# Optimization experiments

Measured on AMD Instinct MI355X. Metric: run time of the kernel, lower is better.

Reference implementation:

```python
import jax, jax.numpy as jnp
import numpy as np

# dims / constants (from init_kwargs and ParamsHP defaults)
N, C, TRS, SPT, BUF = 800, 64, 40, 10, 120
DT = 1e-4                      # step_size
A, OMEGA, G = -0.5, 10.0, 500.0
STD_IN, CY0, Y0_OFF, KG, KI = 100.0, 5.0, 2.0, 5.0, 1.0
T = TRS * SPT                  # total integration steps


def setup_inputs() -> dict:
    key = jax.random.key(0)
    k = jax.random.split(key, 7)
    external = jax.random.normal(k[0], (N, SPT, TRS), dtype=jnp.float32)
    hx = jax.random.uniform(k[1], (N, 2), dtype=jnp.float32)
    hE = jax.random.uniform(k[2], (N, BUF), dtype=jnp.float32)
    sc = jax.random.uniform(k[3], (N, N), dtype=jnp.float32)
    lm = jax.random.normal(k[4], (C, N), dtype=jnp.float32)
    noise_in = jax.random.normal(k[5], (T, N, 2), dtype=jnp.float32)
    # delays[i,j] = int(dist[i,j] / mu), bounded by buffer length
    delays = jax.random.randint(k[6], (N, N), 0, BUF, dtype=jnp.int64)
    return {"external": external, "hx": hx, "hE": hE, "sc": sc,
            "lm": lm, "noise_in": noise_in, "delays": delays}


def reference(external, hx, hE, sc, lm, noise_in, delays):
    # normalized structural connectivity and Laplacian diagonal term
    w = jnp.abs(sc)
    w_n = w / jnp.linalg.norm(w)          # (N,N)
    rowsum = jnp.sum(w_n, axis=1)         # (N,) -> dg = -diag(rowsum)
    jcol = jnp.broadcast_to(jnp.arange(N)[None, :], (N, N))
    # stimulus as (T, N): external is (N, steps_per_TR, TRs_per_window)
    ext = jnp.transpose(external, (2, 1, 0)).reshape(T, N)
    sqdt = jnp.sqrt(DT)

    def step(carry, inp):
        x, y, hEb = carry                 # x,y: (N,), hEb: (N,BUF)
        u, ns = inp                       # u: (N,), ns: (N,2)
        # delayed activity: Ed[i,j] = x_j(t - delays[i,j])
        Ed = hEb[jcol, delays]            # (N,N) irregular gather
        LEd = jnp.sum(w_n * Ed, axis=1)   # connectivity-weighted coupling
        r2 = x * x + y * y
        dx = (A - r2) * x - OMEGA * y + G * (LEd - rowsum * x) + KG * KI * u
        dy = (A - r2) * y + OMEGA * x
        x_new = x + DT * dx + sqdt * STD_IN * ns[:, 0]
        y_new = y + DT * dy + sqdt * STD_IN * ns[:, 1]
        hEb = jnp.concatenate([x_new[:, None], hEb[:, :-1]], axis=1)
        return (x_new, y_new, hEb), x_new

    (xf, yf, hEf), xs = jax.lax.scan(step, (hx[:, 0], hx[:, 1], hE), (ext, noise_in))
    # one EEG sample per TR (state at the last step of each TR)
    x_tr = xs.reshape(TRS, SPT, N)[:, -1, :]   # (TRS, N)
    eeg = CY0 * (x_tr @ lm.T) - Y0_OFF          # leadfield projection (TRS, C)
    return eeg.T                                # (C, TRS)
```

## Files before the change

### kernel.cpp

```cpp
#include <hip/hip_runtime.h>
#include <hip/hip_cooperative_groups.h>

namespace cg = cooperative_groups;

#define N_      800
#define C_      64
#define TRS_    40
#define SPT_    10
#define BUF_    120
#define T_      400
#define STRIDE  528
#define KPL     13
#define SENT    0x7FC00BADu

#define A_F     (-0.5f)
#define OMEGA_F (10.0f)
#define G_F     (500.0f)
#define KGI_F   (5.0f)
#define DT_F    (1e-4f)


__global__ void k_sumsq(const float* __restrict__ sc, float* __restrict__ sumsq) {
    __shared__ float sh[4];
    int tid = threadIdx.x;
    int idx = blockIdx.x * 256 + tid;
    float s = 0.f;
    for (int i = idx; i < N_ * N_; i += 256 * 256) { float v = sc[i]; s += v * v; }
    #pragma unroll
    for (int o = 1; o < 64; o <<= 1) s += __shfl_xor(s, o, 64);
    if ((tid & 63) == 0) sh[tid >> 6] = s;
    __syncthreads();
    if (tid == 0) atomicAdd(sumsq, sh[0] + sh[1] + sh[2] + sh[3]);
}

__global__ void k_detect(const int* __restrict__ dw, int* __restrict__ flag) {
    __shared__ int sh[4];
    int tid = threadIdx.x;
    int v = 0;
    for (int idx = 2 * tid + 1; idx < 800; idx += 512) v |= dw[idx];
    #pragma unroll
    for (int o = 1; o < 64; o <<= 1) v |= __shfl_xor(v, o, 64);
    if ((tid & 63) == 0) sh[tid >> 6] = v;
    __syncthreads();
    if (tid == 0) flag[0] = ((sh[0] | sh[1] | sh[2] | sh[3]) == 0) ? 1 : 0;
}

__global__ void k_init(const float* __restrict__ hE, unsigned int* __restrict__ xh) {
    int idx = blockIdx.x * 256 + threadIdx.x;
    if (idx >= N_ * 520) return;
    int j = idx / 520, s = idx - j * 520;
    unsigned int v = (s < 120) ? __float_as_uint(hE[j * BUF_ + (119 - s)]) : SENT;
    xh[j * STRIDE + s] = v;
}


__global__ void __launch_bounds__(512, 1) k_main(
    const float* __restrict__ sc, const int* __restrict__ dw,
    const float* __restrict__ hx, const float* __restrict__ external,
    const float* __restrict__ noise, const float* __restrict__ lm,
    const float* __restrict__ sumsq, const int* __restrict__ flag,
    unsigned int* __restrict__ xh, float* __restrict__ xtr, float* __restrict__ out)
{
    cg::grid_group grid = cg::this_grid();
    const int lane = threadIdx.x & 63;
    const int wave = (int)((blockIdx.x * 512 + threadIdx.x) >> 6);
    const int i = wave;

    const float inv_norm = 1.0f / sqrtf(*sumsq);
    const int is64 = *flag;

    float w[KPL]; int ofs[KPL];
    float rsum = 0.f;
    #pragma unroll
    for (int k = 0; k < KPL; ++k) {
        int j = k * 64 + lane;
        bool valid = (j < N_);
        int jj = valid ? j : 0;
        int base = i * N_ + jj;
        float wv = valid ? fabsf(sc[base]) * inv_norm : 0.f;
        int di = is64 ? (base << 1) : base;
        int dv = valid ? dw[di] : 119;
        if (!valid) dv = 119;
        w[k] = wv;
        ofs[k] = jj * STRIDE + 119 - dv;
        rsum += wv;
    }
    #pragma unroll
    for (int o = 1; o < 64; o <<= 1) rsum += __shfl_xor(rsum, o, 64);

    float ue[7], n0r[7], n1r[7];
    #pragma unroll
    for (int q = 0; q < 7; ++q) {
        int tp = q * 64 + lane;
        if (tp < T_) {
            int tr = tp / SPT_, sp = tp - tr * SPT_;
            ue[q]  = external[(i * SPT_ + sp) * TRS_ + tr];
            n0r[q] = noise[(tp * N_ + i) * 2 + 0];
            n1r[q] = noise[(tp * N_ + i) * 2 + 1];
        } else { ue[q] = 0.f; n0r[q] = 0.f; n1r[q] = 0.f; }
    }

    float x = hx[2 * i], y = hx[2 * i + 1];

    int t = 0;
    int tmod = 0;
    #pragma unroll
    for (int q = 0; q < 7; ++q) {
        const int tmax = (q == 6) ? (T_ - 6 * 64) : 64;
        #pragma unroll 1
        for (int tt = 0; tt < tmax; ++tt, ++t) {
            unsigned int vv[KPL];
            #pragma unroll
            for (int k = 0; k < KPL; ++k)
                vv[k] = __hip_atomic_load(&xh[ofs[k] + t], __ATOMIC_RELAXED,
                                          __HIP_MEMORY_SCOPE_AGENT);
            int guard = 0;
            while (true) {
                int pend = 0;
                #pragma unroll
                for (int k = 0; k < KPL; ++k) pend |= (vv[k] == SENT) ? 1 : 0;
                if (!__any(pend)) break;
                if (++guard > 100000) break;
                #pragma unroll
                for (int k = 0; k < KPL; ++k)
                    if (vv[k] == SENT)
                        vv[k] = __hip_atomic_load(&xh[ofs[k] + t], __ATOMIC_RELAXED,
                                                  __HIP_MEMORY_SCOPE_AGENT);
            }
            float acc = 0.f;
            #pragma unroll
            for (int k = 0; k < KPL; ++k) acc += w[k] * __uint_as_float(vv[k]);
            #pragma unroll
            for (int o = 1; o < 64; o <<= 1) acc += __shfl_xor(acc, o, 64);

            float u  = __shfl(ue[q],  tt, 64);
            float n0 = __shfl(n0r[q], tt, 64);
            float n1 = __shfl(n1r[q], tt, 64);

            float r2 = x * x + y * y;
            float dx = (A_F - r2) * x - OMEGA_F * y + G_F * (acc - rsum * x) + KGI_F * u;
            float dy = (A_F - r2) * y + OMEGA_F * x;
            x = x + DT_F * dx + n0;
            y = y + DT_F * dy + n1;

            if (lane == 0) {
                __hip_atomic_store(&xh[i * STRIDE + t + 120], __float_as_uint(x),
                                   __ATOMIC_RELAXED, __HIP_MEMORY_SCOPE_AGENT);
                if (tmod == SPT_ - 1) xtr[(t / SPT_) * N_ + i] = x;
            }
            if (++tmod == SPT_) tmod = 0;
        }
    }

    grid.sync();

    for (int o = wave; o < C_ * TRS_; o += 800) {
        int c = o / TRS_, tr = o - c * TRS_;
        float s = 0.f;
        #pragma unroll
        for (int k = 0; k < KPL; ++k) {
            int n = k * 64 + lane;
            if (n < N_) s += xtr[tr * N_ + n] * lm[c * N_ + n];
        }
        #pragma unroll
        for (int o2 = 1; o2 < 64; o2 <<= 1) s += __shfl_xor(s, o2, 64);
        if (lane == 0) out[o] = 5.0f * s - 2.0f;
    }
}


extern "C" void kernel_launch(void* const* d_in, const int* in_sizes, int n_in,
                              void* d_out, int out_size, void* d_ws, size_t ws_size,
                              hipStream_t stream) {
    const float* external = (const float*)d_in[0];
    const float* hx       = (const float*)d_in[1];
    const float* hE       = (const float*)d_in[2];
    const float* sc       = (const float*)d_in[3];
    const float* lm       = (const float*)d_in[4];
    const float* noise    = (const float*)d_in[5];
    const int*   delays   = (const int*)  d_in[6];
    float* out = (float*)d_out;

    float*        sumsq = (float*)d_ws;
    int*          flag  = (int*)d_ws + 1;
    unsigned int* xh    = (unsigned int*)d_ws + 64;
    float*        xtr   = (float*)(xh + N_ * STRIDE);

    hipMemsetAsync(d_ws, 0, 8, stream);
    k_sumsq<<<256, 256, 0, stream>>>(sc, sumsq);
    k_detect<<<1, 256, 0, stream>>>(delays, flag);
    k_init<<<(N_ * 520 + 255) / 256, 256, 0, stream>>>(hE, xh);

    void* args[] = { (void*)&sc, (void*)&delays, (void*)&hx, (void*)&external,
                     (void*)&noise, (void*)&lm, (void*)&sumsq, (void*)&flag,
                     (void*)&xh, (void*)&xtr, (void*)&out };
    hipLaunchCooperativeKernel((const void*)k_main, dim3(100), dim3(512), args, 0, stream);
}
```

Measured before the change: 2.736 ms.

## Batch delayed-history reads over 8-step blocks and split out short-delay couplings

Each row's connections are now split by delay. Connections with delay below 7 go into a compacted per-lane list that is still read step by step with spin-wait atomic loads. All longer delays are prefetched once per 8-step block into register windows: vectorized float4 loads for far delays, atomic loads for mid delays. This is meant to cut per-step global load latency and polling on the serial critical path. It raises register pressure, and far delays now use plain non-atomic loads, which relies on L2 coherence and a sentinel re-check.

```diff
diff --git a/kernel.cpp b/kernel.cpp
--- a/kernel.cpp
+++ b/kernel.cpp
@@ -12,12 +12,16 @@
 #define STRIDE  528
 #define KPL     13
 #define SENT    0x7FC00BADu
+#define FRESH_D 7
+#define MID_D   24
 
 #define A_F     (-0.5f)
 #define OMEGA_F (10.0f)
 #define G_F     (500.0f)
 #define KGI_F   (5.0f)
 #define DT_F    (1e-4f)
+
+#define ALD(p) __hip_atomic_load((p), __ATOMIC_RELAXED, __HIP_MEMORY_SCOPE_AGENT)
 
 
 __global__ void k_sumsq(const float* __restrict__ sc, float* __restrict__ sumsq) {
@@ -63,13 +67,12 @@
 {
     cg::grid_group grid = cg::this_grid();
     const int lane = threadIdx.x & 63;
-    const int wave = (int)((blockIdx.x * 512 + threadIdx.x) >> 6);
-    const int i = wave;
+    const int i = (int)((blockIdx.x * 512 + threadIdx.x) >> 6);
 
     const float inv_norm = 1.0f / sqrtf(*sumsq);
     const int is64 = *flag;
 
-    float w[KPL]; int ofs[KPL];
+    float w[KPL]; int wb[KPL]; int ph[KPL]; int isfar[KPL];
     float rsum = 0.f;
     #pragma unroll
     for (int k = 0; k < KPL; ++k) {
@@ -78,15 +81,41 @@
         int jj = valid ? j : 0;
         int base = i * N_ + jj;
         float wv = valid ? fabsf(sc[base]) * inv_norm : 0.f;
-        int di = is64 ? (base << 1) : base;
-        int dv = valid ? dw[di] : 119;
-        if (!valid) dv = 119;
+        int dv = valid ? dw[is64 ? (base << 1) : base] : 119;
+        rsum += wv;
+        if (dv < FRESH_D) { wv = 0.f; dv = 119; }
         w[k] = wv;
-        ofs[k] = jj * STRIDE + 119 - dv;
-        rsum += wv;
+        if (dv >= MID_D) {
+            int p = (-1 - dv) & 3;
+            ph[k] = p;
+            wb[k] = jj * STRIDE + 120 + (-1 - dv - p);
+            isfar[k] = 1;
+        } else {
+            ph[k] = 0;
+            wb[k] = jj * STRIDE + 119 - dv;
+            isfar[k] = 0;
+        }
     }
     #pragma unroll
     for (int o = 1; o < 64; o <<= 1) rsum += __shfl_xor(rsum, o, 64);
+
+    float fw0 = 0.f, fw1 = 0.f; int fo0 = 0, fo1 = 0;
+    {
+        int c = 0;
+        for (int e = 0; e < N_; ++e) {
+            int be = i * N_ + e;
+            int dv = dw[is64 ? (be << 1) : be];
+            if (dv < FRESH_D) {
+                if ((c & 63) == lane) {
+                    float wv = fabsf(sc[be]) * inv_norm;
+                    int fo = e * STRIDE + 119 - dv;
+                    if (c < 64) { fw0 = wv; fo0 = fo; }
+                    else        { fw1 = wv; fo1 = fo; }
+                }
+                ++c;
+            }
+        }
+    }
 
     float ue[7], n0r[7], n1r[7];
     #pragma unroll
@@ -102,59 +131,102 @@
 
     float x = hx[2 * i], y = hx[2 * i + 1];
 
-    int t = 0;
-    int tmod = 0;
-    #pragma unroll
+    int t = 0, tmod = 0;
+    #pragma unroll 1
     for (int q = 0; q < 7; ++q) {
-        const int tmax = (q == 6) ? (T_ - 6 * 64) : 64;
+        const int nmb = (q == 6) ? 2 : 8;
         #pragma unroll 1
-        for (int tt = 0; tt < tmax; ++tt, ++t) {
-            unsigned int vv[KPL];
+        for (int mb = 0; mb < nmb; ++mb) {
+            const int t0 = t;
+            float win[KPL][12];
+
             #pragma unroll
-            for (int k = 0; k < KPL; ++k)
-                vv[k] = __hip_atomic_load(&xh[ofs[k] + t], __ATOMIC_RELAXED,
-                                          __HIP_MEMORY_SCOPE_AGENT);
+            for (int k = 0; k < KPL; ++k) {
+                if (isfar[k]) {
+                    const float4* fp = reinterpret_cast<const float4*>(
+                        (const float*)xh + wb[k] + t0);
+                    float4 a = fp[0], b = fp[1], cq = fp[2];
+                    win[k][0]=a.x;  win[k][1]=a.y;  win[k][2]=a.z;  win[k][3]=a.w;
+                    win[k][4]=b.x;  win[k][5]=b.y;  win[k][6]=b.z;  win[k][7]=b.w;
+                    win[k][8]=cq.x; win[k][9]=cq.y; win[k][10]=cq.z; win[k][11]=cq.w;
+                } else {
+                    #pragma unroll
+                    for (int s2 = 0; s2 < 8; ++s2)
+                        win[k][s2] = __uint_as_float(ALD(&xh[wb[k] + t0 + s2]));
+                    win[k][8]=0.f; win[k][9]=0.f; win[k][10]=0.f; win[k][11]=0.f;
+                }
+            }
             int guard = 0;
             while (true) {
                 int pend = 0;
                 #pragma unroll
-                for (int k = 0; k < KPL; ++k) pend |= (vv[k] == SENT) ? 1 : 0;
+                for (int k = 0; k < KPL; ++k) {
+                    #pragma unroll
+                    for (int idx = 0; idx < 12; ++idx) {
+                        int need = (idx >= ph[k]) & (idx < ph[k] + 8);
+                        pend |= need & (__float_as_uint(win[k][idx]) == SENT);
+                    }
+                }
                 if (!__any(pend)) break;
-                if (++guard > 100000) break;
-                #pragma unroll
-                for (int k = 0; k < KPL; ++k)
-                    if (vv[k] == SENT)
-                        vv[k] = __hip_atomic_load(&xh[ofs[k] + t], __ATOMIC_RELAXED,
-                                                  __HIP_MEMORY_SCOPE_AGENT);
-            }
-            float acc = 0.f;
+                if (++guard > 200000) break;
+                #pragma unroll
+                for (int k = 0; k < KPL; ++k) {
+                    #pragma unroll
+                    for (int idx = 0; idx < 12; ++idx) {
+                        int need = (idx >= ph[k]) & (idx < ph[k] + 8);
+                        if (need && __float_as_uint(win[k][idx]) == SENT)
+                            win[k][idx] = __uint_as_float(ALD(&xh[wb[k] + t0 + idx]));
+                    }
+                }
+            }
+
             #pragma unroll
-            for (int k = 0; k < KPL; ++k) acc += w[k] * __uint_as_float(vv[k]);
-            #pragma unroll
-            for (int o = 1; o < 64; o <<= 1) acc += __shfl_xor(acc, o, 64);
-
-            float u  = __shfl(ue[q],  tt, 64);
-            float n0 = __shfl(n0r[q], tt, 64);
-            float n1 = __shfl(n1r[q], tt, 64);
-
-            float r2 = x * x + y * y;
-            float dx = (A_F - r2) * x - OMEGA_F * y + G_F * (acc - rsum * x) + KGI_F * u;
-            float dy = (A_F - r2) * y + OMEGA_F * x;
-            x = x + DT_F * dx + n0;
-            y = y + DT_F * dy + n1;
-
-            if (lane == 0) {
-                __hip_atomic_store(&xh[i * STRIDE + t + 120], __float_as_uint(x),
-                                   __ATOMIC_RELAXED, __HIP_MEMORY_SCOPE_AGENT);
-                if (tmod == SPT_ - 1) xtr[(t / SPT_) * N_ + i] = x;
-            }
-            if (++tmod == SPT_) tmod = 0;
+            for (int s = 0; s < 8; ++s) {
+                if (q == 6 && mb == 1 && s >= 8) break;
+                unsigned f0 = ALD(&xh[fo0 + t]);
+                unsigned f1 = ALD(&xh[fo1 + t]);
+                int g2 = 0;
+                while (__any((f0 == SENT) | (f1 == SENT))) {
+                    if (f0 == SENT) f0 = ALD(&xh[fo0 + t]);
+                    if (f1 == SENT) f1 = ALD(&xh[fo1 + t]);
+                    if (++g2 > 200000) break;
+                }
+                float acc = fw0 * __uint_as_float(f0) + fw1 * __uint_as_float(f1);
+                #pragma unroll
+                for (int k = 0; k < KPL; ++k) {
+                    float v01 = (ph[k] & 1) ? win[k][s + 1] : win[k][s + 0];
+                    float v23 = (ph[k] & 1) ? win[k][s + 3] : win[k][s + 2];
+                    float v   = (ph[k] & 2) ? v23 : v01;
+                    acc += w[k] * v;
+                }
+                #pragma unroll
+                for (int o = 1; o < 64; o <<= 1) acc += __shfl_xor(acc, o, 64);
+
+                int tt = mb * 8 + s;
+                float u  = __shfl(ue[q],  tt, 64);
+                float n0 = __shfl(n0r[q], tt, 64);
+                float n1 = __shfl(n1r[q], tt, 64);
+
+                float r2 = x * x + y * y;
+                float dx = (A_F - r2) * x - OMEGA_F * y + G_F * (acc - rsum * x) + KGI_F * u;
+                float dy = (A_F - r2) * y + OMEGA_F * x;
+                x = x + DT_F * dx + n0;
+                y = y + DT_F * dy + n1;
+
+                if (lane == 0) {
+                    __hip_atomic_store(&xh[i * STRIDE + 120 + t], __float_as_uint(x),
+                                       __ATOMIC_RELAXED, __HIP_MEMORY_SCOPE_AGENT);
+                    if (tmod == SPT_ - 1) xtr[(t / SPT_) * N_ + i] = x;
+                }
+                tmod = (tmod == SPT_ - 1) ? 0 : tmod + 1;
+                ++t;
+            }
         }
     }
 
     grid.sync();
 
-    for (int o = wave; o < C_ * TRS_; o += 800) {
+    for (int o = i; o < C_ * TRS_; o += 800) {
         int c = o / TRS_, tr = o - c * TRS_;
         float s = 0.f;
         #pragma unroll
```

New measurement: 9.159 ms. +234.7%, slower.

## Split coupling into near and far delays, batch far-delay loads per 16 steps

Applied to the files above, without the earlier changes.

Connections are split by delay. Those with delay of at least 15 steps have their delayed values already available for a block of 16 steps, so they are read as vectorized float4 windows once per block and accumulated into per-step partial sums. Only near-delay connections still need per-step atomic polling on the shared history. Per-step external and noise inputs are now loaded directly instead of being preloaded and shuffled. This is meant to shorten the serial per-step critical path, at the cost of higher register pressure. Correctness of the far windows relies on the sentinel check, which spins on any entries not yet written.

```diff
diff --git a/kernel.cpp b/kernel.cpp
--- a/kernel.cpp
+++ b/kernel.cpp
@@ -12,12 +12,16 @@
 #define STRIDE  528
 #define KPL     13
 #define SENT    0x7FC00BADu
+#define NEAR_D  15
 
 #define A_F     (-0.5f)
 #define OMEGA_F (10.0f)
 #define G_F     (500.0f)
 #define KGI_F   (5.0f)
 #define DT_F    (1e-4f)
+
+#define ALD(p)    __hip_atomic_load((p), __ATOMIC_RELAXED, __HIP_MEMORY_SCOPE_AGENT)
+#define AST(p,v)  __hip_atomic_store((p), (v), __ATOMIC_RELAXED, __HIP_MEMORY_SCOPE_AGENT)
 
 
 __global__ void k_sumsq(const float* __restrict__ sc, float* __restrict__ sumsq) {
@@ -63,13 +67,12 @@
 {
     cg::grid_group grid = cg::this_grid();
     const int lane = threadIdx.x & 63;
-    const int wave = (int)((blockIdx.x * 512 + threadIdx.x) >> 6);
-    const int i = wave;
+    const int i = (int)((blockIdx.x * 512 + threadIdx.x) >> 6);
 
     const float inv_norm = 1.0f / sqrtf(*sumsq);
     const int is64 = *flag;
 
-    float w[KPL]; int ofs[KPL];
+    float wn[KPL], wf[KPL]; int an[KPL], af[KPL];
     float rsum = 0.f;
     #pragma unroll
     for (int k = 0; k < KPL; ++k) {
@@ -78,64 +81,97 @@
         int jj = valid ? j : 0;
         int base = i * N_ + jj;
         float wv = valid ? fabsf(sc[base]) * inv_norm : 0.f;
-        int di = is64 ? (base << 1) : base;
-        int dv = valid ? dw[di] : 119;
-        if (!valid) dv = 119;
-        w[k] = wv;
-        ofs[k] = jj * STRIDE + 119 - dv;
+        int dv = valid ? dw[is64 ? (base << 1) : base] : 119;
         rsum += wv;
+        bool nearc = valid && (dv < NEAR_D);
+        bool farc  = valid && (dv >= NEAR_D);
+        wn[k] = nearc ? wv : 0.f;
+        wf[k] = farc  ? wv : 0.f;
+        an[k] = jj * STRIDE + 119 - (nearc ? dv : 119);
+        af[k] = jj * STRIDE + 119 - (farc  ? dv : 119);
     }
     #pragma unroll
     for (int o = 1; o < 64; o <<= 1) rsum += __shfl_xor(rsum, o, 64);
 
-    float ue[7], n0r[7], n1r[7];
-    #pragma unroll
-    for (int q = 0; q < 7; ++q) {
-        int tp = q * 64 + lane;
-        if (tp < T_) {
-            int tr = tp / SPT_, sp = tp - tr * SPT_;
-            ue[q]  = external[(i * SPT_ + sp) * TRS_ + tr];
-            n0r[q] = noise[(tp * N_ + i) * 2 + 0];
-            n1r[q] = noise[(tp * N_ + i) * 2 + 1];
-        } else { ue[q] = 0.f; n0r[q] = 0.f; n1r[q] = 0.f; }
-    }
-
     float x = hx[2 * i], y = hx[2 * i + 1];
 
-    int t = 0;
-    int tmod = 0;
-    #pragma unroll
-    for (int q = 0; q < 7; ++q) {
-        const int tmax = (q == 6) ? (T_ - 6 * 64) : 64;
-        #pragma unroll 1
-        for (int tt = 0; tt < tmax; ++tt, ++t) {
-            unsigned int vv[KPL];
-            #pragma unroll
-            for (int k = 0; k < KPL; ++k)
-                vv[k] = __hip_atomic_load(&xh[ofs[k] + t], __ATOMIC_RELAXED,
-                                          __HIP_MEMORY_SCOPE_AGENT);
-            int guard = 0;
+    #pragma unroll 1
+    for (int mb = 0; mb < 25; ++mb) {
+        const int t0 = mb * 16;
+
+        float fps[16];
+        #pragma unroll
+        for (int s = 0; s < 16; ++s) fps[s] = 0.f;
+
+        #pragma unroll
+        for (int k = 0; k < KPL; ++k) {
+            bool fm = (wf[k] != 0.f);
+            int a = af[k] + t0;
+            int p = a & 3;
+            int A = a - p;
+            float4 q0, q1, q2, q3, q4;
+            if (fm) {
+                const float4* f4 = reinterpret_cast<const float4*>((const float*)xh + A);
+                q0 = f4[0]; q1 = f4[1]; q2 = f4[2]; q3 = f4[3]; q4 = f4[4];
+            } else {
+                q0 = q1 = q2 = q3 = q4 = make_float4(0.f, 0.f, 0.f, 0.f);
+            }
+            float win[20] = { q0.x,q0.y,q0.z,q0.w, q1.x,q1.y,q1.z,q1.w,
+                              q2.x,q2.y,q2.z,q2.w, q3.x,q3.y,q3.z,q3.w,
+                              q4.x,q4.y,q4.z,q4.w };
+            int g = 0;
             while (true) {
                 int pend = 0;
                 #pragma unroll
+                for (int z = 0; z < 20; ++z)
+                    pend |= (int)((z >= p) & (z < p + 16) &
+                                  (__float_as_uint(win[z]) == SENT));
+                if (!__any(pend)) break;
+                if (++g > 1000000) break;
+                #pragma unroll
+                for (int z = 0; z < 20; ++z)
+                    if ((z >= p) && (z < p + 16) && __float_as_uint(win[z]) == SENT)
+                        win[z] = __uint_as_float(ALD(&xh[A + z]));
+            }
+            float wk = wf[k];
+            #pragma unroll
+            for (int s = 0; s < 16; ++s) {
+                float v01 = (p & 1) ? win[s + 1] : win[s];
+                float v23 = (p & 1) ? win[s + 3] : win[s + 2];
+                float v   = (p & 2) ? v23 : v01;
+                fps[s] += wk * v;
+            }
+        }
+
+        #pragma unroll
+        for (int s = 0; s < 16; ++s) {
+            const int t = t0 + s;
+            int tr = (t * 205) >> 11;
+            int sp = t - tr * 10;
+            float u  = external[(i * SPT_ + sp) * TRS_ + tr];
+            float n0 = noise[(t * N_ + i) * 2 + 0];
+            float n1 = noise[(t * N_ + i) * 2 + 1];
+
+            unsigned vv[KPL];
+            #pragma unroll
+            for (int k = 0; k < KPL; ++k)
+                vv[k] = (wn[k] != 0.f) ? ALD(&xh[an[k] + t]) : 0u;
+            int g = 0;
+            while (true) {
+                int pend = 0;
+                #pragma unroll
                 for (int k = 0; k < KPL; ++k) pend |= (vv[k] == SENT) ? 1 : 0;
                 if (!__any(pend)) break;
-                if (++guard > 100000) break;
+                if (++g > 1000000) break;
                 #pragma unroll
                 for (int k = 0; k < KPL; ++k)
-                    if (vv[k] == SENT)
-                        vv[k] = __hip_atomic_load(&xh[ofs[k] + t], __ATOMIC_RELAXED,
-                                                  __HIP_MEMORY_SCOPE_AGENT);
-            }
-            float acc = 0.f;
-            #pragma unroll
-            for (int k = 0; k < KPL; ++k) acc += w[k] * __uint_as_float(vv[k]);
+                    if (vv[k] == SENT) vv[k] = ALD(&xh[an[k] + t]);
+            }
+            float acc = fps[s];
+            #pragma unroll
+            for (int k = 0; k < KPL; ++k) acc += wn[k] * __uint_as_float(vv[k]);
             #pragma unroll
             for (int o = 1; o < 64; o <<= 1) acc += __shfl_xor(acc, o, 64);
-
-            float u  = __shfl(ue[q],  tt, 64);
-            float n0 = __shfl(n0r[q], tt, 64);
-            float n1 = __shfl(n1r[q], tt, 64);
 
             float r2 = x * x + y * y;
             float dx = (A_F - r2) * x - OMEGA_F * y + G_F * (acc - rsum * x) + KGI_F * u;
@@ -144,17 +180,15 @@
             y = y + DT_F * dy + n1;
 
             if (lane == 0) {
-                __hip_atomic_store(&xh[i * STRIDE + t + 120], __float_as_uint(x),
-                                   __ATOMIC_RELAXED, __HIP_MEMORY_SCOPE_AGENT);
-                if (tmod == SPT_ - 1) xtr[(t / SPT_) * N_ + i] = x;
-            }
-            if (++tmod == SPT_) tmod = 0;
+                AST(&xh[i * STRIDE + 120 + t], __float_as_uint(x));
+                if (sp == SPT_ - 1) xtr[tr * N_ + i] = x;
+            }
         }
     }
 
     grid.sync();
 
-    for (int o = wave; o < C_ * TRS_; o += 800) {
+    for (int o = i; o < C_ * TRS_; o += 800) {
         int c = o / TRS_, tr = o - c * TRS_;
         float s = 0.f;
         #pragma unroll
```

New measurement: 2.727 ms. Within noise of the previous version (-0.3%).
